# Kernel optimization log

Measured on AMD Instinct MI355X. Metric: run time of the kernel, lower is better.

The kernel has to match this reference:

```python
import jax, jax.numpy as jnp
import numpy as np

B, H, S = 256, 128, 2048

def setup_inputs() -> dict:
    key = jax.random.key(0)
    ks = jax.random.split(key, 8)
    static_embedding = jax.random.normal(ks[0], (B, H, S), dtype=jnp.float32)
    dynamic_embedding = jax.random.normal(ks[1], (B, S, H), dtype=jnp.float32)
    decoder_output = jax.random.normal(ks[2], (B, H, 1), dtype=jnp.float32)
    mask = jax.random.randint(ks[3], (B, S), 0, 2).astype(bool)
    # xavier-uniform-ish init scales
    lim_v = float(np.sqrt(6.0 / (1 + H)))
    lim_W = float(np.sqrt(6.0 / (H + 3 * H)))
    lim_W2 = float(np.sqrt(6.0 / (H + 2 * H)))
    v = jax.random.uniform(ks[4], (H,), minval=-lim_v, maxval=lim_v, dtype=jnp.float32)
    W = jax.random.uniform(ks[5], (H, 3 * H), minval=-lim_W, maxval=lim_W, dtype=jnp.float32)
    v2 = jax.random.uniform(ks[6], (H,), minval=-lim_v, maxval=lim_v, dtype=jnp.float32)
    W2 = jax.random.uniform(ks[7], (H, 2 * H), minval=-lim_W2, maxval=lim_W2, dtype=jnp.float32)
    return {"static_embedding": static_embedding, "dynamic_embedding": dynamic_embedding,
            "decoder_output": decoder_output, "mask": mask,
            "v": v, "W": W, "v2": v2, "W2": W2}


def reference(static_embedding, dynamic_embedding, decoder_output, mask, v, W, v2, W2):
    b, h, s = static_embedding.shape
    dec = jnp.broadcast_to(decoder_output, (b, h, s))               # [B,H,S]
    hidden = jnp.concatenate(
        [static_embedding, jnp.swapaxes(dynamic_embedding, 1, 2), dec], axis=1)  # [B,3H,S]
    # stage 1: additive scoring  v^T tanh(W @ hidden)
    t1 = jnp.tanh(jnp.einsum('hk,bks->bhs', W, hidden))             # [B,H,S]
    attns = jnp.einsum('h,bhs->bs', v, t1)                          # [B,S]
    enc_attn = jax.nn.softmax(attns, axis=1)                        # [B,S]
    # context over static embeddings
    context = jnp.einsum('bs,bhs->bh', enc_attn, static_embedding)  # [B,H]
    energy = jnp.concatenate(
        [static_embedding, jnp.broadcast_to(context[:, :, None], (b, h, s))], axis=1)  # [B,2H,S]
    # stage 2
    t2 = jnp.tanh(jnp.einsum('hk,bks->bhs', W2, energy))            # [B,H,S]
    probs = jnp.einsum('h,bhs->bs', v2, t2)                         # [B,S]
    probs = jnp.where(mask, -jnp.inf, probs)
    return jax.nn.softmax(probs, axis=1)
```

## Files before the change

### kernel.cpp

```cpp
#include <hip/hip_runtime.h>
#include <stdint.h>
#include <math.h>

#define B_ 256
#define H_ 128
#define S_ 2048

typedef __attribute__((ext_vector_type(8))) short short8;
typedef __attribute__((ext_vector_type(4))) float f32x4;

typedef const __attribute__((address_space(1))) void gvoid_t;
typedef __attribute__((address_space(3))) void lvoid_t;

__device__ __forceinline__ unsigned short f2bf(float f) {
  uint32_t u = __builtin_bit_cast(uint32_t, f);
  u += 0x7fffu + ((u >> 16) & 1u);
  return (unsigned short)(u >> 16);
}

__device__ __forceinline__ float tanh_fast(float x) {
  float ax = fabsf(x);
  float e = __expf(-2.0f * ax);
  float t = (1.0f - e) / (1.0f + e);
  return copysignf(t, x);
}

#define WS_NEED 4718592u
#define WST_OFF 8388608u
#define WS_T_NEED (WST_OFF + (size_t)B_ * (S_/16) * 4 * 64 * 8 * 2)

__global__ __launch_bounds__(256) void prep_wfrags(
    const float* __restrict__ W, const float* __restrict__ W2,
    unsigned short* __restrict__ wsA) {
  int idx = blockIdx.x * 256 + threadIdx.x;
  if (idx >= 24 * 4 * 64 * 8) return;
  int j = idx & 7;
  int lane = (idx >> 3) & 63;
  int t = (idx >> 9) & 3;
  int tile = idx >> 11;
  int li = lane & 15;
  int k = t * 32 + (lane >> 4) * 8 + j;
  float val;
  if (tile < 8)        val = W[(tile * 16 + li) * 384 + k];
  else if (tile < 16)  val = W2[((tile - 8) * 16 + li) * 256 + k];
  else                 val = W[((tile - 16) * 16 + li) * 384 + 128 + k];
  wsA[idx] = f2bf(val);
}

__global__ __launch_bounds__(128) void prep_c1(
    const float* __restrict__ W, const float* __restrict__ dec,
    float* __restrict__ c1) {
  int b = blockIdx.x;
  int h = threadIdx.x;
  __shared__ float sdec[H_];
  sdec[h] = dec[b * H_ + h];
  __syncthreads();
  const float* wr = W + h * 384 + 256;
  float acc = 0.f;
  #pragma unroll 4
  for (int k = 0; k < 128; ++k) acc += wr[k] * sdec[k];
  c1[b * H_ + h] = acc;
}

__global__ void detect_mask(const unsigned char* __restrict__ mb, int* __restrict__ flag) {
  __shared__ int sGT1, sNZ;
  if (threadIdx.x == 0) { sGT1 = 0; sNZ = 0; }
  __syncthreads();
  int gt1 = 0, nz = 0;
  for (int i = threadIdx.x; i < 8192; i += 256) {
    unsigned char c = mb[i];
    if (c > 1) gt1 = 1;
    if ((i & 3) && c) nz = 1;
  }
  if (gt1) atomicOr(&sGT1, 1);
  if (nz)  atomicOr(&sNZ, 1);
  __syncthreads();
  if (threadIdx.x == 0) *flag = sGT1 ? 2 : (sNZ ? 1 : 0);
}

__global__ __launch_bounds__(256) void stage1(
    const float* __restrict__ sEmb, const float* __restrict__ dEmb,
    const unsigned short* __restrict__ wsA, const float* __restrict__ c1,
    const float* __restrict__ v, float* __restrict__ attns,
    unsigned short* __restrict__ wsT) {
  const int b = blockIdx.y;
  const int tid = threadIdx.x;
  const int lane = tid & 63, w = tid >> 6, g = lane >> 4, li = lane & 15;
  __shared__ float sS[128 * 64];
  __shared__ float sD[64 * 128];
  __shared__ unsigned short frag[4][8][512];
  __shared__ float spart[256];
  __shared__ float sc1[H_], sv[H_];

  const size_t sbase = (size_t)b * H_ * S_;
  const size_t dbase = (size_t)b * S_ * H_;
  const int sblk = blockIdx.x * 512;

  short8 aW[2][4], aB[2][4];
  #pragma unroll
  for (int mm = 0; mm < 2; ++mm)
    #pragma unroll
    for (int t = 0; t < 4; ++t) {
      aW[mm][t] = *(const short8*)(wsA + (size_t)(((2 * w + mm) * 4 + t) * 64 + lane) * 8);
      aB[mm][t] = *(const short8*)(wsA + (size_t)(((16 + 2 * w + mm) * 4 + t) * 64 + lane) * 8);
    }

  if (tid < 128) { sc1[tid] = c1[b * H_ + tid]; sv[tid] = v[tid]; }

  auto stage = [&](int soff) {
    int lrow = lane >> 4, lcol4 = 4 * (lane & 15);
    #pragma unroll
    for (int i = 0; i < 8; ++i) {
      int r = 32 * w + 4 * i + lrow;
      int gcol = lcol4 ^ (((r >> 3) & 3) << 3);
      const float* src = sEmb + sbase + (size_t)r * S_ + soff + gcol;
      __builtin_amdgcn_global_load_lds((gvoid_t*)src, (lvoid_t*)&sS[(32 * w + 4 * i) * 64],
                                       16, 0, 0);
    }
    int lrow2 = lane >> 5, lch = lane & 31;
    #pragma unroll
    for (int i = 0; i < 8; ++i) {
      int s = 16 * w + 2 * i + lrow2;
      int sch = lch ^ (s & 7);
      const float* src = dEmb + dbase + (size_t)(soff + s) * H_ + 4 * sch;
      __builtin_amdgcn_global_load_lds((gvoid_t*)src, (lvoid_t*)&sD[(16 * w + 2 * i) * 128],
                                       16, 0, 0);
    }
  };
  stage(sblk);

  const int colA = (16 * w + li) ^ (g << 3);
  const int srow = 16 * w + li;

  for (int c = 0; c < 8; ++c) {
    const int soff = sblk + c * 64;
    __syncthreads();
    #pragma unroll
    for (int t = 0; t < 4; ++t) {
      short8 bS;
      #pragma unroll
      for (int j = 0; j < 8; ++j)
        bS[j] = (short)f2bf(sS[(32 * t + 8 * g + j) * 64 + colA]);
      f32x4 d0 = *(const f32x4*)&sD[srow * 128 + 4 * ((8 * t + 2 * g + 0) ^ (li & 7))];
      f32x4 d1 = *(const f32x4*)&sD[srow * 128 + 4 * ((8 * t + 2 * g + 1) ^ (li & 7))];
      short8 bD;
      bD[0] = (short)f2bf(d0.x); bD[1] = (short)f2bf(d0.y);
      bD[2] = (short)f2bf(d0.z); bD[3] = (short)f2bf(d0.w);
      bD[4] = (short)f2bf(d1.x); bD[5] = (short)f2bf(d1.y);
      bD[6] = (short)f2bf(d1.z); bD[7] = (short)f2bf(d1.w);
      *(short8*)&frag[w][t][lane * 8] = bS;
      *(short8*)&frag[w][4 + t][lane * 8] = bD;
      if (wsT)
        *(short8*)&wsT[(((size_t)b * (S_ / 16) + (soff >> 4) + w) * 4 + t) * 512 + lane * 8] = bS;
    }
    __syncthreads();
    if (c + 1 < 8) stage(soff + 64);

    f32x4 acc[4][2];
    #pragma unroll
    for (int st = 0; st < 4; ++st) { acc[st][0] = (f32x4)0.0f; acc[st][1] = (f32x4)0.0f; }
    #pragma unroll
    for (int st = 0; st < 4; ++st)
      #pragma unroll
      for (int t = 0; t < 4; ++t) {
        short8 bS = *(const short8*)&frag[st][t][lane * 8];
        short8 bD = *(const short8*)&frag[st][4 + t][lane * 8];
        acc[st][0] = __builtin_amdgcn_mfma_f32_16x16x32_bf16(aW[0][t], bS, acc[st][0], 0, 0, 0);
        acc[st][1] = __builtin_amdgcn_mfma_f32_16x16x32_bf16(aW[1][t], bS, acc[st][1], 0, 0, 0);
        acc[st][0] = __builtin_amdgcn_mfma_f32_16x16x32_bf16(aB[0][t], bD, acc[st][0], 0, 0, 0);
        acc[st][1] = __builtin_amdgcn_mfma_f32_16x16x32_bf16(aB[1][t], bD, acc[st][1], 0, 0, 0);
      }

    #pragma unroll
    for (int st = 0; st < 4; ++st) {
      float part = 0.f;
      #pragma unroll
      for (int mm = 0; mm < 2; ++mm)
        #pragma unroll
        for (int r = 0; r < 4; ++r) {
          int h = 32 * w + 16 * mm + 4 * g + r;
          part += sv[h] * tanh_fast(acc[st][mm][r] + sc1[h]);
        }
      part += __shfl_xor(part, 16);
      part += __shfl_xor(part, 32);
      if (lane < 16) spart[w * 64 + st * 16 + li] = part;
    }
    __syncthreads();
    if (tid < 64)
      attns[(size_t)b * S_ + soff + tid] =
          spart[tid] + spart[64 + tid] + spart[128 + tid] + spart[192 + tid];
  }
}

__global__ __launch_bounds__(256) void kmid_a(
    const float* __restrict__ attns, const float* __restrict__ sEmb,
    float* __restrict__ ctx) {
  int q = blockIdx.x, b = blockIdx.y;
  int tid = threadIdx.x, lane = tid & 63, w = tid >> 6;
  __shared__ float p[S_];
  __shared__ float wred[4];
  __shared__ float sred;

  float a[8];
  #pragma unroll
  for (int i = 0; i < 8; ++i) a[i] = attns[(size_t)b * S_ + i * 256 + tid];
  float mx = a[0];
  #pragma unroll
  for (int i = 1; i < 8; ++i) mx = fmaxf(mx, a[i]);
  #pragma unroll
  for (int off = 32; off >= 1; off >>= 1) mx = fmaxf(mx, __shfl_xor(mx, off));
  if (lane == 0) wred[w] = mx;
  __syncthreads();
  if (tid == 0) sred = fmaxf(fmaxf(wred[0], wred[1]), fmaxf(wred[2], wred[3]));
  __syncthreads();
  mx = sred;
  __syncthreads();
  float sum = 0.f;
  #pragma unroll
  for (int i = 0; i < 8; ++i) {
    float e = __expf(a[i] - mx);
    p[i * 256 + tid] = e;
    sum += e;
  }
  #pragma unroll
  for (int off = 32; off >= 1; off >>= 1) sum += __shfl_xor(sum, off);
  if (lane == 0) wred[w] = sum;
  __syncthreads();
  if (tid == 0) sred = 1.0f / (wred[0] + wred[1] + wred[2] + wred[3]);
  __syncthreads();
  float inv = sred;

  #pragma unroll
  for (int hh = 0; hh < 8; ++hh) {
    int h = q * 32 + w * 8 + hh;
    const f32x4* xp = (const f32x4*)(sEmb + (size_t)b * H_ * S_ + (size_t)h * S_);
    float av = 0.f;
    #pragma unroll
    for (int it = 0; it < 8; ++it) {
      f32x4 x = xp[it * 64 + lane];
      f32x4 pp = *(const f32x4*)&p[(it * 64 + lane) * 4];
      av += x.x * pp.x + x.y * pp.y + x.z * pp.z + x.w * pp.w;
    }
    #pragma unroll
    for (int off = 32; off >= 1; off >>= 1) av += __shfl_xor(av, off);
    if (lane == 0) ctx[b * H_ + h] = av * inv;
  }
}

__global__ __launch_bounds__(128) void kmid_b(
    const float* __restrict__ W2, const float* __restrict__ ctx,
    float* __restrict__ c2) {
  int b = blockIdx.x;
  int h = threadIdx.x;
  __shared__ float sc[H_];
  sc[h] = ctx[b * H_ + h];
  __syncthreads();
  const float* wr = W2 + h * 256 + 128;
  float acc = 0.f;
  #pragma unroll 4
  for (int k = 0; k < 128; ++k) acc += wr[k] * sc[k];
  c2[b * H_ + h] = acc;
}

__global__ __launch_bounds__(256) void stage2T(
    const unsigned short* __restrict__ wsT, const unsigned short* __restrict__ wsA,
    const float* __restrict__ c2, const float* __restrict__ v2,
    const unsigned char* __restrict__ mask8, const int* __restrict__ flag,
    float* __restrict__ score) {
  const int b = blockIdx.y;
  const int tid = threadIdx.x;
  const int lane = tid & 63, w = tid >> 6, g = lane >> 4, li = lane & 15;
  __shared__ unsigned short frag[4][4][512];
  __shared__ float spart[256];
  __shared__ float sc2[H_], sv2[H_];

  const int schunk = blockIdx.x * 64;

  short8 aW[2][4];
  #pragma unroll
  for (int mm = 0; mm < 2; ++mm)
    #pragma unroll
    for (int t = 0; t < 4; ++t)
      aW[mm][t] = *(const short8*)(wsA + (size_t)(((8 + 2 * w + mm) * 4 + t) * 64 + lane) * 8);

  {
    size_t base = ((size_t)b * (S_ / 16) + (schunk >> 4) + w) * 4 * 512;
    #pragma unroll
    for (int t = 0; t < 4; ++t) {
      const unsigned short* src = wsT + base + t * 512 + lane * 8;
      __builtin_amdgcn_global_load_lds((gvoid_t*)src, (lvoid_t*)&frag[w][t][0], 16, 0, 0);
    }
  }

  if (tid < 128) { sc2[tid] = c2[b * H_ + tid]; sv2[tid] = v2[tid]; }
  __syncthreads();

  f32x4 acc[4][2];
  #pragma unroll
  for (int st = 0; st < 4; ++st) { acc[st][0] = (f32x4)0.0f; acc[st][1] = (f32x4)0.0f; }
  #pragma unroll
  for (int st = 0; st < 4; ++st)
    #pragma unroll
    for (int t = 0; t < 4; ++t) {
      short8 bS = *(const short8*)&frag[st][t][lane * 8];
      acc[st][0] = __builtin_amdgcn_mfma_f32_16x16x32_bf16(aW[0][t], bS, acc[st][0], 0, 0, 0);
      acc[st][1] = __builtin_amdgcn_mfma_f32_16x16x32_bf16(aW[1][t], bS, acc[st][1], 0, 0, 0);
    }

  #pragma unroll
  for (int st = 0; st < 4; ++st) {
    float part = 0.f;
    #pragma unroll
    for (int mm = 0; mm < 2; ++mm)
      #pragma unroll
      for (int r = 0; r < 4; ++r) {
        int h = 32 * w + 16 * mm + 4 * g + r;
        part += sv2[h] * tanh_fast(acc[st][mm][r] + sc2[h]);
      }
    part += __shfl_xor(part, 16);
    part += __shfl_xor(part, 32);
    if (lane < 16) spart[w * 64 + st * 16 + li] = part;
  }
  __syncthreads();

  if (tid < 64) {
    float tot = spart[tid] + spart[64 + tid] + spart[128 + tid] + spart[192 + tid];
    size_t mi = (size_t)b * S_ + schunk + tid;
    int f = *flag;
    bool msk;
    if (f == 1)      msk = mask8[mi] != 0;
    else if (f == 2) msk = ((const float*)mask8)[mi] != 0.0f;
    else             msk = ((const int*)mask8)[mi] != 0;
    score[mi] = msk ? -INFINITY : tot;
  }
}

__global__ __launch_bounds__(256) void stage2F(
    const float* __restrict__ sEmb, const unsigned short* __restrict__ wsA,
    const float* __restrict__ c2, const float* __restrict__ v2,
    const unsigned char* __restrict__ mask8, const int* __restrict__ flag,
    float* __restrict__ score) {
  int b = blockIdx.y;
  int tid = threadIdx.x;
  int lane = tid & 63, w = tid >> 6, g = lane >> 4, li = lane & 15;
  __shared__ float sS[128 * 64];
  __shared__ float sc2[H_], sv2[H_];
  __shared__ float spart[256];

  const int schunk = blockIdx.x * 64;
  const size_t sbase = (size_t)b * H_ * S_;

  short8 aW[2][4];
  #pragma unroll
  for (int mm = 0; mm < 2; ++mm)
    #pragma unroll
    for (int t = 0; t < 4; ++t)
      aW[mm][t] = *(const short8*)(wsA + (size_t)(((8 + 2 * w + mm) * 4 + t) * 64 + lane) * 8);

  {
    int lrow = lane >> 4, lcol4 = 4 * (lane & 15);
    #pragma unroll
    for (int i = 0; i < 8; ++i) {
      int r = 32 * w + 4 * i + lrow;
      int gcol = lcol4 ^ (((r >> 3) & 3) << 3);
      const float* src = sEmb + sbase + (size_t)r * S_ + schunk + gcol;
      __builtin_amdgcn_global_load_lds((gvoid_t*)src, (lvoid_t*)&sS[(32 * w + 4 * i) * 64],
                                       16, 0, 0);
    }
  }

  if (tid < 128) { sc2[tid] = c2[b * H_ + tid]; sv2[tid] = v2[tid]; }
  __syncthreads();

  f32x4 acc[4][2];
  #pragma unroll
  for (int st = 0; st < 4; ++st) { acc[st][0] = (f32x4)0.0f; acc[st][1] = (f32x4)0.0f; }

  #pragma unroll
  for (int st = 0; st < 4; ++st) {
    const int colA = (16 * st + li) ^ (g << 3);
    #pragma unroll
    for (int t = 0; t < 4; ++t) {
      short8 bS;
      #pragma unroll
      for (int j = 0; j < 8; ++j)
        bS[j] = (short)f2bf(sS[(32 * t + 8 * g + j) * 64 + colA]);
      acc[st][0] = __builtin_amdgcn_mfma_f32_16x16x32_bf16(aW[0][t], bS, acc[st][0], 0, 0, 0);
      acc[st][1] = __builtin_amdgcn_mfma_f32_16x16x32_bf16(aW[1][t], bS, acc[st][1], 0, 0, 0);
    }
  }

  #pragma unroll
  for (int st = 0; st < 4; ++st) {
    float part = 0.f;
    #pragma unroll
    for (int mm = 0; mm < 2; ++mm)
      #pragma unroll
      for (int r = 0; r < 4; ++r) {
        int h = 32 * w + 16 * mm + 4 * g + r;
        part += sv2[h] * tanh_fast(acc[st][mm][r] + sc2[h]);
      }
    part += __shfl_xor(part, 16);
    part += __shfl_xor(part, 32);
    if (lane < 16) spart[w * 64 + st * 16 + li] = part;
  }
  __syncthreads();

  if (tid < 64) {
    float tot = spart[tid] + spart[64 + tid] + spart[128 + tid] + spart[192 + tid];
    size_t mi = (size_t)b * S_ + schunk + tid;
    int f = *flag;
    bool msk;
    if (f == 1)      msk = mask8[mi] != 0;
    else if (f == 2) msk = ((const float*)mask8)[mi] != 0.0f;
    else             msk = ((const int*)mask8)[mi] != 0;
    score[mi] = msk ? -INFINITY : tot;
  }
}

__global__ __launch_bounds__(256) void ksoftmax(
    const float* __restrict__ score, float* __restrict__ out) {
  int b = blockIdx.x;
  int tid = threadIdx.x, lane = tid & 63, w = tid >> 6;
  __shared__ float wred[4];
  __shared__ float sred;
  float a[8];
  #pragma unroll
  for (int i = 0; i < 8; ++i) a[i] = score[(size_t)b * S_ + i * 256 + tid];
  float mx = a[0];
  #pragma unroll
  for (int i = 1; i < 8; ++i) mx = fmaxf(mx, a[i]);
  #pragma unroll
  for (int off = 32; off >= 1; off >>= 1) mx = fmaxf(mx, __shfl_xor(mx, off));
  if (lane == 0) wred[w] = mx;
  __syncthreads();
  if (tid == 0) sred = fmaxf(fmaxf(wred[0], wred[1]), fmaxf(wred[2], wred[3]));
  __syncthreads();
  mx = sred;
  __syncthreads();
  float e[8];
  float sum = 0.f;
  #pragma unroll
  for (int i = 0; i < 8; ++i) { e[i] = __expf(a[i] - mx); sum += e[i]; }
  #pragma unroll
  for (int off = 32; off >= 1; off >>= 1) sum += __shfl_xor(sum, off);
  if (lane == 0) wred[w] = sum;
  __syncthreads();
  if (tid == 0) sred = 1.0f / (wred[0] + wred[1] + wred[2] + wred[3]);
  __syncthreads();
  float inv = sred;
  #pragma unroll
  for (int i = 0; i < 8; ++i) out[(size_t)b * S_ + i * 256 + tid] = e[i] * inv;
}

extern "C" void kernel_launch(void* const* d_in, const int* in_sizes, int n_in,
                              void* d_out, int out_size, void* d_ws, size_t ws_size,
                              hipStream_t stream) {
  (void)in_sizes; (void)n_in; (void)out_size;
  if (ws_size < WS_NEED) return;
  const float* sEmb = (const float*)d_in[0];
  const float* dEmb = (const float*)d_in[1];
  const float* dec  = (const float*)d_in[2];
  const unsigned char* mask = (const unsigned char*)d_in[3];
  const float* v    = (const float*)d_in[4];
  const float* W    = (const float*)d_in[5];
  const float* v2   = (const float*)d_in[6];
  const float* W2   = (const float*)d_in[7];

  char* ws = (char*)d_ws;
  unsigned short* wsA = (unsigned short*)(ws);
  int*   flag  = (int*)  (ws + 114688);
  float* c1    = (float*)(ws + 131072);
  float* c2    = (float*)(ws + 262144);
  float* ctx   = (float*)(ws + 393216);
  float* attns = (float*)(ws + 524288);
  float* score = (float*)(ws + 2621440);
  bool useT = (ws_size >= WS_T_NEED);
  unsigned short* wsT = useT ? (unsigned short*)(ws + WST_OFF) : nullptr;

  prep_wfrags<<<192, 256, 0, stream>>>(W, W2, wsA);
  prep_c1<<<B_, 128, 0, stream>>>(W, dec, c1);
  detect_mask<<<1, 256, 0, stream>>>(mask, flag);
  stage1<<<dim3(4, B_), 256, 0, stream>>>(sEmb, dEmb, wsA, c1, v, attns, wsT);
  kmid_a<<<dim3(4, B_), 256, 0, stream>>>(attns, sEmb, ctx);
  kmid_b<<<B_, 128, 0, stream>>>(W2, ctx, c2);
  if (useT)
    stage2T<<<dim3(32, B_), 256, 0, stream>>>(wsT, wsA, c2, v2, mask, flag, score);
  else
    stage2F<<<dim3(32, B_), 256, 0, stream>>>(sEmb, wsA, c2, v2, mask, flag, score);
  ksoftmax<<<B_, 256, 0, stream>>>(score, (float*)d_out);
}
```

Measured before the change: 286.5 us.

## Fuse softmax, context, stage-2 scoring and final softmax into one per-batch kernel

Adds a fuse2 kernel, one 512-thread block per batch row. It performs the first softmax, computes the context from the cached bf16 static tiles in wsT, builds c2, runs the stage-2 MFMA scoring with masking, and finishes with the output softmax, replacing four launches. Stage1 now loads the dynamic embedding straight into registers instead of staging it through LDS. It packs bf16 with v_cvt_pk_bf16_f32, uses a cheaper exp2/rcp tanh, and defers the attns store past the next barrier. Risks: the context is now computed from bf16-rounded static data, and only 256 blocks run for the fused stage, which lowers parallelism.

```diff
diff --git a/kernel.cpp b/kernel.cpp
--- a/kernel.cpp
+++ b/kernel.cpp
@@ -8,6 +8,7 @@
 
 typedef __attribute__((ext_vector_type(8))) short short8;
 typedef __attribute__((ext_vector_type(4))) float f32x4;
+typedef __attribute__((ext_vector_type(4))) unsigned int u32x4;
 
 typedef const __attribute__((address_space(1))) void gvoid_t;
 typedef __attribute__((address_space(3))) void lvoid_t;
@@ -18,11 +19,20 @@
   return (unsigned short)(u >> 16);
 }
 
-__device__ __forceinline__ float tanh_fast(float x) {
-  float ax = fabsf(x);
-  float e = __expf(-2.0f * ax);
-  float t = (1.0f - e) / (1.0f + e);
-  return copysignf(t, x);
+__device__ __forceinline__ uint32_t cvtpk(float lo, float hi) {
+  uint32_t r;
+  asm("v_cvt_pk_bf16_f32 %0, %1, %2" : "=v"(r) : "v"(lo), "v"(hi));
+  return r;
+}
+
+__device__ __forceinline__ float bf2f(unsigned short u) {
+  return __builtin_bit_cast(float, (uint32_t)u << 16);
+}
+
+__device__ __forceinline__ float tanh5(float x) {
+  float e = __builtin_amdgcn_exp2f(x * 2.8853900817779268f);
+  float r = __builtin_amdgcn_rcpf(1.0f + e);
+  return fmaf(-2.0f, r, 1.0f);
 }
 
 #define WS_NEED 4718592u
@@ -87,7 +97,6 @@
   const int tid = threadIdx.x;
   const int lane = tid & 63, w = tid >> 6, g = lane >> 4, li = lane & 15;
   __shared__ float sS[128 * 64];
-  __shared__ float sD[64 * 128];
   __shared__ unsigned short frag[4][8][512];
   __shared__ float spart[256];
   __shared__ float sc1[H_], sv[H_];
@@ -104,11 +113,10 @@
       aW[mm][t] = *(const short8*)(wsA + (size_t)(((2 * w + mm) * 4 + t) * 64 + lane) * 8);
       aB[mm][t] = *(const short8*)(wsA + (size_t)(((16 + 2 * w + mm) * 4 + t) * 64 + lane) * 8);
     }
-
   if (tid < 128) { sc1[tid] = c1[b * H_ + tid]; sv[tid] = v[tid]; }
 
-  auto stage = [&](int soff) {
-    int lrow = lane >> 4, lcol4 = 4 * (lane & 15);
+  const int lrow = lane >> 4, lcol4 = 4 * (lane & 15);
+  auto stageS = [&](int soff) {
     #pragma unroll
     for (int i = 0; i < 8; ++i) {
       int r = 32 * w + 4 * i + lrow;
@@ -117,44 +125,51 @@
       __builtin_amdgcn_global_load_lds((gvoid_t*)src, (lvoid_t*)&sS[(32 * w + 4 * i) * 64],
                                        16, 0, 0);
     }
-    int lrow2 = lane >> 5, lch = lane & 31;
-    #pragma unroll
-    for (int i = 0; i < 8; ++i) {
-      int s = 16 * w + 2 * i + lrow2;
-      int sch = lch ^ (s & 7);
-      const float* src = dEmb + dbase + (size_t)(soff + s) * H_ + 4 * sch;
-      __builtin_amdgcn_global_load_lds((gvoid_t*)src, (lvoid_t*)&sD[(16 * w + 2 * i) * 128],
-                                       16, 0, 0);
-    }
   };
-  stage(sblk);
+  f32x4 dv[8];
+  auto loadD = [&](int soff) {
+    const float* dr = dEmb + dbase + (size_t)(soff + 16 * w + li) * H_ + 8 * g;
+    #pragma unroll
+    for (int t = 0; t < 4; ++t) {
+      dv[2 * t]     = *(const f32x4*)(dr + 32 * t);
+      dv[2 * t + 1] = *(const f32x4*)(dr + 32 * t + 4);
+    }
+  };
+
+  stageS(sblk);
+  loadD(sblk);
 
   const int colA = (16 * w + li) ^ (g << 3);
-  const int srow = 16 * w + li;
 
   for (int c = 0; c < 8; ++c) {
     const int soff = sblk + c * 64;
     __syncthreads();
+    if (c > 0 && tid < 64)
+      attns[(size_t)b * S_ + soff - 64 + tid] =
+          spart[tid] + spart[64 + tid] + spart[128 + tid] + spart[192 + tid];
+
     #pragma unroll
     for (int t = 0; t < 4; ++t) {
-      short8 bS;
-      #pragma unroll
-      for (int j = 0; j < 8; ++j)
-        bS[j] = (short)f2bf(sS[(32 * t + 8 * g + j) * 64 + colA]);
-      f32x4 d0 = *(const f32x4*)&sD[srow * 128 + 4 * ((8 * t + 2 * g + 0) ^ (li & 7))];
-      f32x4 d1 = *(const f32x4*)&sD[srow * 128 + 4 * ((8 * t + 2 * g + 1) ^ (li & 7))];
-      short8 bD;
-      bD[0] = (short)f2bf(d0.x); bD[1] = (short)f2bf(d0.y);
-      bD[2] = (short)f2bf(d0.z); bD[3] = (short)f2bf(d0.w);
-      bD[4] = (short)f2bf(d1.x); bD[5] = (short)f2bf(d1.y);
-      bD[6] = (short)f2bf(d1.z); bD[7] = (short)f2bf(d1.w);
+      const int rb = (32 * t + 8 * g) * 64 + colA;
+      uint32_t s0 = cvtpk(sS[rb], sS[rb + 64]);
+      uint32_t s1 = cvtpk(sS[rb + 128], sS[rb + 192]);
+      uint32_t s2 = cvtpk(sS[rb + 256], sS[rb + 320]);
+      uint32_t s3 = cvtpk(sS[rb + 384], sS[rb + 448]);
+      u32x4 us = {s0, s1, s2, s3};
+      short8 bS = __builtin_bit_cast(short8, us);
+      uint32_t d0 = cvtpk(dv[2 * t].x, dv[2 * t].y);
+      uint32_t d1 = cvtpk(dv[2 * t].z, dv[2 * t].w);
+      uint32_t d2 = cvtpk(dv[2 * t + 1].x, dv[2 * t + 1].y);
+      uint32_t d3 = cvtpk(dv[2 * t + 1].z, dv[2 * t + 1].w);
+      u32x4 ud = {d0, d1, d2, d3};
+      short8 bD = __builtin_bit_cast(short8, ud);
       *(short8*)&frag[w][t][lane * 8] = bS;
       *(short8*)&frag[w][4 + t][lane * 8] = bD;
       if (wsT)
         *(short8*)&wsT[(((size_t)b * (S_ / 16) + (soff >> 4) + w) * 4 + t) * 512 + lane * 8] = bS;
     }
     __syncthreads();
-    if (c + 1 < 8) stage(soff + 64);
+    if (c + 1 < 8) { stageS(soff + 64); loadD(soff + 64); }
 
     f32x4 acc[4][2];
     #pragma unroll
@@ -179,17 +194,224 @@
         #pragma unroll
         for (int r = 0; r < 4; ++r) {
           int h = 32 * w + 16 * mm + 4 * g + r;
-          part += sv[h] * tanh_fast(acc[st][mm][r] + sc1[h]);
+          part += sv[h] * tanh5(acc[st][mm][r] + sc1[h]);
         }
       part += __shfl_xor(part, 16);
       part += __shfl_xor(part, 32);
       if (lane < 16) spart[w * 64 + st * 16 + li] = part;
     }
-    __syncthreads();
-    if (tid < 64)
-      attns[(size_t)b * S_ + soff + tid] =
-          spart[tid] + spart[64 + tid] + spart[128 + tid] + spart[192 + tid];
-  }
+  }
+  __syncthreads();
+  if (tid < 64)
+    attns[(size_t)b * S_ + sblk + 448 + tid] =
+        spart[tid] + spart[64 + tid] + spart[128 + tid] + spart[192 + tid];
+}
+
+__global__ __launch_bounds__(512) void fuse2(
+    const float* __restrict__ attns, const unsigned short* __restrict__ wsT,
+    const unsigned short* __restrict__ wsA, const float* __restrict__ W2,
+    const float* __restrict__ v2, const unsigned char* __restrict__ mask8,
+    const int* __restrict__ flag, float* __restrict__ out) {
+  const int b = blockIdx.x;
+  const int tid = threadIdx.x;
+  const int lane = tid & 63, wv = tid >> 6, g = lane >> 4, li = lane & 15;
+  __shared__ float buf[S_];
+  __shared__ float sctx[8][H_];
+  __shared__ float2 sq[H_];
+  __shared__ float wred[8];
+  __shared__ float sred;
+
+  const size_t pbase = (size_t)b * (S_ / 16);
+
+  float a[4];
+  #pragma unroll
+  for (int i = 0; i < 4; ++i) a[i] = attns[(size_t)b * S_ + i * 512 + tid];
+  float mx = fmaxf(fmaxf(a[0], a[1]), fmaxf(a[2], a[3]));
+  #pragma unroll
+  for (int off = 32; off >= 1; off >>= 1) mx = fmaxf(mx, __shfl_xor(mx, off));
+  if (lane == 0) wred[wv] = mx;
+  __syncthreads();
+  if (tid == 0) {
+    float m = wred[0];
+    #pragma unroll
+    for (int i = 1; i < 8; ++i) m = fmaxf(m, wred[i]);
+    sred = m;
+  }
+  __syncthreads();
+  mx = sred;
+  __syncthreads();
+  float sum = 0.f;
+  #pragma unroll
+  for (int i = 0; i < 4; ++i) {
+    float e = __expf(a[i] - mx);
+    buf[i * 512 + tid] = e;
+    sum += e;
+  }
+  #pragma unroll
+  for (int off = 32; off >= 1; off >>= 1) sum += __shfl_xor(sum, off);
+  if (lane == 0) wred[wv] = sum;
+  __syncthreads();
+  if (tid == 0) {
+    float s = 0.f;
+    #pragma unroll
+    for (int i = 0; i < 8; ++i) s += wred[i];
+    sred = 1.0f / s;
+  }
+  __syncthreads();
+  const float inv1 = sred;
+  __syncthreads();
+
+  float hacc[4][8];
+  #pragma unroll
+  for (int t = 0; t < 4; ++t)
+    #pragma unroll
+    for (int j = 0; j < 8; ++j) hacc[t][j] = 0.f;
+  short8 cur[4];
+  #pragma unroll
+  for (int t = 0; t < 4; ++t)
+    cur[t] = *(const short8*)&wsT[((pbase + wv) * 4 + t) * 512 + lane * 8];
+  for (int stile = wv; stile < 128; stile += 8) {
+    short8 nxt[4];
+    const bool more = (stile + 8) < 128;
+    if (more) {
+      #pragma unroll
+      for (int t = 0; t < 4; ++t)
+        nxt[t] = *(const short8*)&wsT[((pbase + stile + 8) * 4 + t) * 512 + lane * 8];
+    }
+    float pw = buf[stile * 16 + li];
+    #pragma unroll
+    for (int t = 0; t < 4; ++t)
+      #pragma unroll
+      for (int j = 0; j < 8; ++j)
+        hacc[t][j] = fmaf(pw, bf2f((unsigned short)cur[t][j]), hacc[t][j]);
+    if (more) {
+      #pragma unroll
+      for (int t = 0; t < 4; ++t) cur[t] = nxt[t];
+    }
+  }
+  #pragma unroll
+  for (int t = 0; t < 4; ++t)
+    #pragma unroll
+    for (int j = 0; j < 8; ++j) {
+      float x = hacc[t][j];
+      x += __shfl_xor(x, 1); x += __shfl_xor(x, 2);
+      x += __shfl_xor(x, 4); x += __shfl_xor(x, 8);
+      hacc[t][j] = x;
+    }
+  if (li == 0) {
+    #pragma unroll
+    for (int t = 0; t < 4; ++t)
+      #pragma unroll
+      for (int j = 0; j < 8; ++j)
+        sctx[wv][32 * t + 8 * g + j] = hacc[t][j];
+  }
+  __syncthreads();
+
+  if (tid < 128) {
+    float cx = 0.f;
+    #pragma unroll
+    for (int q = 0; q < 8; ++q) cx += sctx[q][tid];
+    sctx[0][tid] = cx * inv1;
+  }
+  __syncthreads();
+  if (tid < 128) {
+    const float* wr = W2 + tid * 256 + 128;
+    float c2v = 0.f;
+    #pragma unroll 4
+    for (int k = 0; k < 128; ++k) c2v += wr[k] * sctx[0][k];
+    sq[tid] = make_float2(c2v, v2[tid]);
+  }
+  __syncthreads();
+
+  short8 aW[8][4];
+  #pragma unroll
+  for (int m = 0; m < 8; ++m)
+    #pragma unroll
+    for (int t = 0; t < 4; ++t)
+      aW[m][t] = *(const short8*)(wsA + (size_t)(((8 + m) * 4 + t) * 64 + lane) * 8);
+  const int f = *flag;
+
+  short8 bcur[4];
+  #pragma unroll
+  for (int t = 0; t < 4; ++t)
+    bcur[t] = *(const short8*)&wsT[((pbase + wv) * 4 + t) * 512 + lane * 8];
+  for (int stile = wv; stile < 128; stile += 8) {
+    short8 bnxt[4];
+    const bool more = (stile + 8) < 128;
+    if (more) {
+      #pragma unroll
+      for (int t = 0; t < 4; ++t)
+        bnxt[t] = *(const short8*)&wsT[((pbase + stile + 8) * 4 + t) * 512 + lane * 8];
+    }
+    f32x4 acc[8];
+    #pragma unroll
+    for (int m = 0; m < 8; ++m) acc[m] = (f32x4)0.0f;
+    #pragma unroll
+    for (int t = 0; t < 4; ++t)
+      #pragma unroll
+      for (int m = 0; m < 8; ++m)
+        acc[m] = __builtin_amdgcn_mfma_f32_16x16x32_bf16(aW[m][t], bcur[t], acc[m], 0, 0, 0);
+    float part = 0.f;
+    #pragma unroll
+    for (int m = 0; m < 8; ++m)
+      #pragma unroll
+      for (int r = 0; r < 4; ++r) {
+        float2 q = sq[16 * m + 4 * g + r];
+        part += q.y * tanh5(acc[m][r] + q.x);
+      }
+    part += __shfl_xor(part, 16);
+    part += __shfl_xor(part, 32);
+    if (lane < 16) {
+      int s = stile * 16 + li;
+      size_t mi = (size_t)b * S_ + s;
+      bool msk;
+      if (f == 1)      msk = mask8[mi] != 0;
+      else if (f == 2) msk = ((const float*)mask8)[mi] != 0.0f;
+      else             msk = ((const int*)mask8)[mi] != 0;
+      buf[s] = msk ? -INFINITY : part;
+    }
+    if (more) {
+      #pragma unroll
+      for (int t = 0; t < 4; ++t) bcur[t] = bnxt[t];
+    }
+  }
+  __syncthreads();
+
+  float s4[4];
+  #pragma unroll
+  for (int i = 0; i < 4; ++i) s4[i] = buf[i * 512 + tid];
+  float mx2 = fmaxf(fmaxf(s4[0], s4[1]), fmaxf(s4[2], s4[3]));
+  #pragma unroll
+  for (int off = 32; off >= 1; off >>= 1) mx2 = fmaxf(mx2, __shfl_xor(mx2, off));
+  if (lane == 0) wred[wv] = mx2;
+  __syncthreads();
+  if (tid == 0) {
+    float m = wred[0];
+    #pragma unroll
+    for (int i = 1; i < 8; ++i) m = fmaxf(m, wred[i]);
+    sred = m;
+  }
+  __syncthreads();
+  mx2 = sred;
+  __syncthreads();
+  float e4[4];
+  float sum2 = 0.f;
+  #pragma unroll
+  for (int i = 0; i < 4; ++i) { e4[i] = __expf(s4[i] - mx2); sum2 += e4[i]; }
+  #pragma unroll
+  for (int off = 32; off >= 1; off >>= 1) sum2 += __shfl_xor(sum2, off);
+  if (lane == 0) wred[wv] = sum2;
+  __syncthreads();
+  if (tid == 0) {
+    float s = 0.f;
+    #pragma unroll
+    for (int i = 0; i < 8; ++i) s += wred[i];
+    sred = 1.0f / s;
+  }
+  __syncthreads();
+  const float inv2 = sred;
+  #pragma unroll
+  for (int i = 0; i < 4; ++i) out[(size_t)b * S_ + i * 512 + tid] = e4[i] * inv2;
 }
 
 __global__ __launch_bounds__(256) void kmid_a(
@@ -200,7 +422,6 @@
   __shared__ float p[S_];
   __shared__ float wred[4];
   __shared__ float sred;
-
   float a[8];
   #pragma unroll
   for (int i = 0; i < 8; ++i) a[i] = attns[(size_t)b * S_ + i * 256 + tid];
@@ -229,7 +450,6 @@
   if (tid == 0) sred = 1.0f / (wred[0] + wred[1] + wred[2] + wred[3]);
   __syncthreads();
   float inv = sred;
-
   #pragma unroll
   for (int hh = 0; hh < 8; ++hh) {
     int h = q * 32 + w * 8 + hh;
@@ -260,79 +480,6 @@
   #pragma unroll 4
   for (int k = 0; k < 128; ++k) acc += wr[k] * sc[k];
   c2[b * H_ + h] = acc;
-}
-
-__global__ __launch_bounds__(256) void stage2T(
-    const unsigned short* __restrict__ wsT, const unsigned short* __restrict__ wsA,
-    const float* __restrict__ c2, const float* __restrict__ v2,
-    const unsigned char* __restrict__ mask8, const int* __restrict__ flag,
-    float* __restrict__ score) {
-  const int b = blockIdx.y;
-  const int tid = threadIdx.x;
-  const int lane = tid & 63, w = tid >> 6, g = lane >> 4, li = lane & 15;
-  __shared__ unsigned short frag[4][4][512];
-  __shared__ float spart[256];
-  __shared__ float sc2[H_], sv2[H_];
-
-  const int schunk = blockIdx.x * 64;
-
-  short8 aW[2][4];
-  #pragma unroll
-  for (int mm = 0; mm < 2; ++mm)
-    #pragma unroll
-    for (int t = 0; t < 4; ++t)
-      aW[mm][t] = *(const short8*)(wsA + (size_t)(((8 + 2 * w + mm) * 4 + t) * 64 + lane) * 8);
-
-  {
-    size_t base = ((size_t)b * (S_ / 16) + (schunk >> 4) + w) * 4 * 512;
-    #pragma unroll
-    for (int t = 0; t < 4; ++t) {
-      const unsigned short* src = wsT + base + t * 512 + lane * 8;
-      __builtin_amdgcn_global_load_lds((gvoid_t*)src, (lvoid_t*)&frag[w][t][0], 16, 0, 0);
-    }
-  }
-
-  if (tid < 128) { sc2[tid] = c2[b * H_ + tid]; sv2[tid] = v2[tid]; }
-  __syncthreads();
-
-  f32x4 acc[4][2];
-  #pragma unroll
-  for (int st = 0; st < 4; ++st) { acc[st][0] = (f32x4)0.0f; acc[st][1] = (f32x4)0.0f; }
-  #pragma unroll
-  for (int st = 0; st < 4; ++st)
-    #pragma unroll
-    for (int t = 0; t < 4; ++t) {
-      short8 bS = *(const short8*)&frag[st][t][lane * 8];
-      acc[st][0] = __builtin_amdgcn_mfma_f32_16x16x32_bf16(aW[0][t], bS, acc[st][0], 0, 0, 0);
-      acc[st][1] = __builtin_amdgcn_mfma_f32_16x16x32_bf16(aW[1][t], bS, acc[st][1], 0, 0, 0);
-    }
-
-  #pragma unroll
-  for (int st = 0; st < 4; ++st) {
-    float part = 0.f;
-    #pragma unroll
-    for (int mm = 0; mm < 2; ++mm)
-      #pragma unroll
-      for (int r = 0; r < 4; ++r) {
-        int h = 32 * w + 16 * mm + 4 * g + r;
-        part += sv2[h] * tanh_fast(acc[st][mm][r] + sc2[h]);
-      }
-    part += __shfl_xor(part, 16);
-    part += __shfl_xor(part, 32);
-    if (lane < 16) spart[w * 64 + st * 16 + li] = part;
-  }
-  __syncthreads();
-
-  if (tid < 64) {
-    float tot = spart[tid] + spart[64 + tid] + spart[128 + tid] + spart[192 + tid];
-    size_t mi = (size_t)b * S_ + schunk + tid;
-    int f = *flag;
-    bool msk;
-    if (f == 1)      msk = mask8[mi] != 0;
-    else if (f == 2) msk = ((const float*)mask8)[mi] != 0.0f;
-    else             msk = ((const int*)mask8)[mi] != 0;
-    score[mi] = msk ? -INFINITY : tot;
-  }
 }
 
 __global__ __launch_bounds__(256) void stage2F(
@@ -346,17 +493,14 @@
   __shared__ float sS[128 * 64];
   __shared__ float sc2[H_], sv2[H_];
   __shared__ float spart[256];
-
   const int schunk = blockIdx.x * 64;
   const size_t sbase = (size_t)b * H_ * S_;
-
   short8 aW[2][4];
   #pragma unroll
   for (int mm = 0; mm < 2; ++mm)
     #pragma unroll
     for (int t = 0; t < 4; ++t)
       aW[mm][t] = *(const short8*)(wsA + (size_t)(((8 + 2 * w + mm) * 4 + t) * 64 + lane) * 8);
-
   {
     int lrow = lane >> 4, lcol4 = 4 * (lane & 15);
     #pragma unroll
@@ -368,14 +512,11 @@
                                        16, 0, 0);
     }
   }
-
   if (tid < 128) { sc2[tid] = c2[b * H_ + tid]; sv2[tid] = v2[tid]; }
   __syncthreads();
-
   f32x4 acc[4][2];
   #pragma unroll
   for (int st = 0; st < 4; ++st) { acc[st][0] = (f32x4)0.0f; acc[st][1] = (f32x4)0.0f; }
-
   #pragma unroll
   for (int st = 0; st < 4; ++st) {
     const int colA = (16 * st + li) ^ (g << 3);
@@ -389,7 +530,6 @@
       acc[st][1] = __builtin_amdgcn_mfma_f32_16x16x32_bf16(aW[1][t], bS, acc[st][1], 0, 0, 0);
     }
   }
-
   #pragma unroll
   for (int st = 0; st < 4; ++st) {
     float part = 0.f;
@@ -398,14 +538,13 @@
       #pragma unroll
       for (int r = 0; r < 4; ++r) {
         int h = 32 * w + 16 * mm + 4 * g + r;
-        part += sv2[h] * tanh_fast(acc[st][mm][r] + sc2[h]);
+        part += sv2[h] * tanh5(acc[st][mm][r] + sc2[h]);
       }
     part += __shfl_xor(part, 16);
     part += __shfl_xor(part, 32);
     if (lane < 16) spart[w * 64 + st * 16 + li] = part;
   }
   __syncthreads();
-
   if (tid < 64) {
     float tot = spart[tid] + spart[64 + tid] + spart[128 + tid] + spart[192 + tid];
     size_t mi = (size_t)b * S_ + schunk + tid;
@@ -482,11 +621,12 @@
   prep_c1<<<B_, 128, 0, stream>>>(W, dec, c1);
   detect_mask<<<1, 256, 0, stream>>>(mask, flag);
   stage1<<<dim3(4, B_), 256, 0, stream>>>(sEmb, dEmb, wsA, c1, v, attns, wsT);
-  kmid_a<<<dim3(4, B_), 256, 0, stream>>>(attns, sEmb, ctx);
-  kmid_b<<<B_, 128, 0, stream>>>(W2, ctx, c2);
-  if (useT)
-    stage2T<<<dim3(32, B_), 256, 0, stream>>>(wsT, wsA, c2, v2, mask, flag, score);
-  else
+  if (useT) {
+    fuse2<<<B_, 512, 0, stream>>>(attns, wsT, wsA, W2, v2, mask, flag, (float*)d_out);
+  } else {
+    kmid_a<<<dim3(4, B_), 256, 0, stream>>>(attns, sEmb, ctx);
+    kmid_b<<<B_, 128, 0, stream>>>(W2, ctx, c2);
     stage2F<<<dim3(32, B_), 256, 0, stream>>>(sEmb, wsA, c2, v2, mask, flag, score);
-  ksoftmax<<<B_, 256, 0, stream>>>(score, (float*)d_out);
-}
+    ksoftmax<<<B_, 256, 0, stream>>>(score, (float*)d_out);
+  }
+}
```

After: 229.9 us. 19.8% less time.
